# Kernel tuning notes

Measured on AMD Instinct MI355X. Metric: run time of the kernel, lower is better.

Reference implementation:

```python
import jax, jax.numpy as jnp
import numpy as np

# Config constants (mirrors VQConfig)
N_CODEBOOKS = 4
NUM_EMBS = 512
EMB_DIM = 32
NUM_LATENTS = 64
DECAY = 0.999
COMMITMENT_COST = 0.25
EPSILON = 1e-05
BATCH = 1024


def setup_inputs() -> dict:
    key = jax.random.key(0)
    k1, k2 = jax.random.split(key)
    x = jax.random.normal(k1, (BATCH, N_CODEBOOKS * EMB_DIM * NUM_LATENTS), dtype=jnp.float32)
    # embedding.uniform_(-1/M*5, 1/M*5)
    lim = 5.0 / NUM_EMBS
    embedding = jax.random.uniform(k2, (N_CODEBOOKS, NUM_EMBS, EMB_DIM), dtype=jnp.float32,
                                   minval=-lim, maxval=lim)
    ema_count = jnp.zeros((N_CODEBOOKS, NUM_EMBS), dtype=jnp.float32)
    ema_weight = embedding  # clone of embedding at init
    return {"x": x, "embedding": embedding, "ema_count": ema_count, "ema_weight": ema_weight}


def reference(x, embedding, ema_count, ema_weight):
    N, M, D = embedding.shape
    B = x.shape[0]
    L = x.shape[1] // (N * D)  # num_discrete_latents (H dim; W = 1)
    T = B * L  # flattened positions per codebook

    # x.view(B, N*D, L, 1).view(B, N, D, H, W).permute(1,0,3,4,2) -> [N,B,L,1,D]
    xr = x.reshape(B, N, D, L, 1).transpose(1, 0, 3, 4, 2)
    x_flat = jax.lax.stop_gradient(xr).reshape(N, T, D)

    e_sq = jnp.sum(embedding ** 2, axis=2)                       # [N, M]
    x_sq = jnp.sum(x_flat ** 2, axis=2, keepdims=True)           # [N, T, 1]
    xe = jnp.einsum('ntd,nmd->ntm', x_flat, embedding)           # [N, T, M]
    distances = e_sq[:, None, :] + x_sq - 2.0 * xe
    indices = jnp.argmin(distances, axis=-1)                     # [N, T] int

    # gather: quantized[n, t] = embedding[n, indices[n, t]]
    quantized = jnp.take_along_axis(embedding, indices[..., None], axis=1)  # [N,T,D]
    quantized_r = quantized.reshape(N, B, L, 1, D)

    # one-hot sums without materializing one-hot: scatter-add via segment_sum
    flat_idx = (indices + jnp.arange(N, dtype=indices.dtype)[:, None] * M).reshape(-1)
    counts = jax.ops.segment_sum(jnp.ones((N * T,), jnp.float32), flat_idx,
                                 num_segments=N * M).reshape(N, M)
    dw = jax.ops.segment_sum(x_flat.reshape(N * T, D), flat_idx,
                             num_segments=N * M).reshape(N, M, D)

    # EMA updates (training branch)
    new_ema_count = DECAY * ema_count + (1.0 - DECAY) * counts
    n_tot = jnp.sum(new_ema_count, axis=-1, keepdims=True)
    new_ema_count = (new_ema_count + EPSILON) / (n_tot + M * EPSILON) * n_tot
    new_ema_weight = DECAY * ema_weight + (1.0 - DECAY) * dw
    new_embedding = new_ema_weight / new_ema_count[..., None]

    # commitment loss + straight-through estimator
    e_latent_loss = jnp.mean((xr - jax.lax.stop_gradient(quantized_r)) ** 2)
    loss = COMMITMENT_COST * e_latent_loss
    quantized_st = jax.lax.stop_gradient(quantized_r) + xr - jax.lax.stop_gradient(xr)

    # perplexity
    avg_probs = counts / T                                       # [N, M]
    perplexity = jnp.exp(-jnp.sum(avg_probs * jnp.log(avg_probs + 1e-10), axis=-1))
    perplexity_sum = jnp.sum(perplexity)

    # [N,B,L,1,D] -> permute(1,0,4,2,3) -> [B,N,D,L,1] -> flatten
    z_q = quantized_st.transpose(1, 0, 4, 2, 3).reshape(B, N * D * L)
    indices_out = indices.reshape(N, B, L, 1).transpose(1, 0, 2, 3)  # [B,N,L,1]

    return (z_q, loss, perplexity_sum, indices_out,
            new_embedding, new_ema_count, new_ema_weight)
```

## Files before the change

### kernel.cpp

```cpp
#include <hip/hip_runtime.h>

#define NCB 4
#define M 512
#define D 32
#define L 64
#define B 1024
#define XS (NCB * D * L)
#define HALF_M 256

#define ZQ_OFF   0
#define LOSS_OFF 8388608
#define PERP_OFF 8388609
#define IDX_OFF  8388610
#define NEMB_OFF 8650754
#define NEC_OFF  8716290
#define NWE_OFF  8718338

#define WS_COUNTS 0
#define WS_DW     2048
#define WS_SSE    67584
#define WS_FLOATS (WS_SSE + 1)

#define NP_SUM32(sq, res) do {                                              \
    float r0=(sq)[0], r1=(sq)[1], r2=(sq)[2], r3=(sq)[3];                   \
    float r4=(sq)[4], r5=(sq)[5], r6=(sq)[6], r7=(sq)[7];                   \
    r0 += (sq)[8];  r1 += (sq)[9];  r2 += (sq)[10]; r3 += (sq)[11];         \
    r4 += (sq)[12]; r5 += (sq)[13]; r6 += (sq)[14]; r7 += (sq)[15];         \
    r0 += (sq)[16]; r1 += (sq)[17]; r2 += (sq)[18]; r3 += (sq)[19];         \
    r4 += (sq)[20]; r5 += (sq)[21]; r6 += (sq)[22]; r7 += (sq)[23];         \
    r0 += (sq)[24]; r1 += (sq)[25]; r2 += (sq)[26]; r3 += (sq)[27];         \
    r4 += (sq)[28]; r5 += (sq)[29]; r6 += (sq)[30]; r7 += (sq)[31];         \
    (res) = ((r0 + r1) + (r2 + r3)) + ((r4 + r5) + (r6 + r7));              \
} while (0)

__global__ __launch_bounds__(256) void vq_main(
    const float* __restrict__ x, const float* __restrict__ emb,
    float* __restrict__ out, float* __restrict__ ws)
{
#pragma clang fp contract(off)
    __shared__ float s_emb[HALF_M * D];
    __shared__ float s_esq[HALF_M];

    const int tid = threadIdx.x;
    const int lane = tid & 63;
    const int bid = blockIdx.x;
    const int n  = bid >> 7;
    const int t0 = (bid & 127) << 9;
    const float* __restrict__ embn = emb + n * (M * D);

    float xr[2][D];
    int tt[2];
#pragma unroll
    for (int j = 0; j < 2; ++j) {
        const int t = t0 + j * 256 + tid;
        tt[j] = t;
        const int b = t >> 6, l = t & 63;
        const float* xp = x + (size_t)b * XS + n * (D * L) + l;
#pragma unroll
        for (int d = 0; d < D; ++d) xr[j][d] = xp[d * L];
    }

    float xsq[2];
#pragma unroll
    for (int j = 0; j < 2; ++j) {
        float sq[D];
#pragma unroll
        for (int d = 0; d < D; ++d) sq[d] = xr[j][d] * xr[j][d];
        NP_SUM32(sq, xsq[j]);
    }

    float best[2] = {3.4e38f, 3.4e38f};
    int   bidx[2] = {0, 0};

    for (int half = 0; half < 2; ++half) {
        if (half) __syncthreads();
        const float4* src = (const float4*)(embn + half * HALF_M * D);
        float4* dst = (float4*)s_emb;
#pragma unroll
        for (int k = 0; k < 8; ++k) dst[tid + k * 256] = src[tid + k * 256];
        __syncthreads();
        {
            float sq[D];
#pragma unroll
            for (int d = 0; d < D; ++d) {
                const float e = s_emb[tid * D + d];
                sq[d] = e * e;
            }
            NP_SUM32(sq, s_esq[tid]);
        }
        __syncthreads();

        for (int mm = 0; mm < HALF_M; ++mm) {
            float ee[D];
            {
                const float4* e4 = (const float4*)(s_emb + mm * D);
#pragma unroll
                for (int q = 0; q < 8; ++q) {
                    const float4 v = e4[q];
                    ee[q*4+0] = v.x; ee[q*4+1] = v.y; ee[q*4+2] = v.z; ee[q*4+3] = v.w;
                }
            }
            const float es = s_esq[mm];
            const int m = half * HALF_M + mm;
#pragma unroll
            for (int j = 0; j < 2; ++j) {
                float l[4];
#pragma unroll
                for (int il = 0; il < 4; ++il) {
                    float c;
                    c = xr[j][12+il] * ee[12+il];
                    c = xr[j][ 8+il] * ee[ 8+il] + c;
                    c = xr[j][ 4+il] * ee[ 4+il] + c;
                    c = xr[j][ 0+il] * ee[ 0+il] + c;
                    c = xr[j][28+il] * ee[28+il] + c;
                    c = xr[j][24+il] * ee[24+il] + c;
                    c = xr[j][20+il] * ee[20+il] + c;
                    c = xr[j][16+il] * ee[16+il] + c;
                    l[il] = c;
                }
                const float xe   = (l[0] + l[1]) + (l[2] + l[3]);
                const float a1   = es + xsq[j];
                const float dist = a1 - 2.f * xe;
                if (dist < best[j]) { best[j] = dist; bidx[j] = m; }
            }
        }
    }

    float sse = 0.f;
#pragma unroll
    for (int j = 0; j < 2; ++j) {
        const int t = tt[j], b = t >> 6, l = t & 63;
        const float* q = embn + bidx[j] * D;
        float* zq = out + ZQ_OFF + (size_t)b * XS + n * (D * L) + l;
#pragma unroll
        for (int d = 0; d < D; ++d) {
            const float qv = q[d];
            zq[d * L] = qv;
            const float diff = xr[j][d] - qv;
            sse = fmaf(diff, diff, sse);
        }
        out[IDX_OFF + ((size_t)b * NCB + n) * L + l] = (float)bidx[j];
        unsafeAtomicAdd(&ws[WS_COUNTS + n * M + bidx[j]], 1.0f);
        float* dwp = ws + WS_DW + (size_t)(n * M + bidx[j]) * D;
#pragma unroll
        for (int d = 0; d < D; ++d) unsafeAtomicAdd(&dwp[d], xr[j][d]);
    }

#pragma unroll
    for (int off = 32; off > 0; off >>= 1) sse += __shfl_down(sse, off, 64);
    if (lane == 0) unsafeAtomicAdd(&ws[WS_SSE], sse);
}

__global__ __launch_bounds__(256) void vq_finalize(
    const float* __restrict__ ema_count, const float* __restrict__ ema_weight,
    const float* __restrict__ ws, float* __restrict__ out)
{
    const int n = blockIdx.x, tid = threadIdx.x;
    __shared__ float s_nec[M];
    __shared__ float s_red[16];

    float pre[2], tot = 0.f, ent = 0.f;
#pragma unroll
    for (int k = 0; k < 2; ++k) {
        const int m = tid + k * 256;
        const float c = ws[WS_COUNTS + n * M + m];
        pre[k] = 0.999f * ema_count[n * M + m] + 0.001f * c;
        tot += pre[k];
        const float p = c * (1.f / 65536.f);
        ent += p * logf(p + 1e-10f);
    }
#pragma unroll
    for (int off = 32; off > 0; off >>= 1) {
        tot += __shfl_down(tot, off, 64);
        ent += __shfl_down(ent, off, 64);
    }
    const int w = tid >> 6;
    if ((tid & 63) == 0) { s_red[w] = tot; s_red[8 + w] = ent; }
    __syncthreads();
    tot = s_red[0] + s_red[1] + s_red[2] + s_red[3];
    ent = s_red[8] + s_red[9] + s_red[10] + s_red[11];

    if (tid == 0) unsafeAtomicAdd(&out[PERP_OFF], expf(-ent));
    if (n == 0 && tid == 0) out[LOSS_OFF] = 0.25f * ws[WS_SSE] * (1.f / 8388608.f);

#pragma unroll
    for (int k = 0; k < 2; ++k) {
        const int m = tid + k * 256;
        const float nec = (pre[k] + 1e-5f) / (tot + M * 1e-5f) * tot;
        out[NEC_OFF + n * M + m] = nec;
        s_nec[m] = nec;
    }
    __syncthreads();

    for (int e = tid; e < M * D; e += 256) {
        const int m = e >> 5;
        const float wv = 0.999f * ema_weight[n * (M * D) + e] + 0.001f * ws[WS_DW + n * (M * D) + e];
        out[NWE_OFF + n * (M * D) + e] = wv;
        out[NEMB_OFF + n * (M * D) + e] = wv / s_nec[m];
    }
}

extern "C" void kernel_launch(void* const* d_in, const int* in_sizes, int n_in,
                              void* d_out, int out_size, void* d_ws, size_t ws_size,
                              hipStream_t stream) {
    const float* x          = (const float*)d_in[0];
    const float* embedding  = (const float*)d_in[1];
    const float* ema_count  = (const float*)d_in[2];
    const float* ema_weight = (const float*)d_in[3];
    float* out = (float*)d_out;
    float* ws  = (float*)d_ws;

    hipMemsetAsync(ws, 0, WS_FLOATS * sizeof(float), stream);
    hipMemsetAsync((char*)d_out + (size_t)LOSS_OFF * sizeof(float), 0, 2 * sizeof(float), stream);

    vq_main<<<dim3(512), dim3(256), 0, stream>>>(x, embedding, out, ws);
    vq_finalize<<<dim3(NCB), dim3(256), 0, stream>>>(ema_count, ema_weight, ws, out);
}
```

Measured before the change: 892.6 us.

## Use fast FMA distance search with top-two tracking and exact refinement of near-ties

Replaces the contract-off distance loop with an FMA-based score (||e||^2 - 2x·e, dropping the constant ||x||^2) and tracks both the best and second-best score per point. Points whose top two scores lie within a small epsilon are recomputed wave-cooperatively with the original exact arithmetic, keeping the argmin bit-compatible with the reference. Each thread now handles one point instead of two, the grid is doubled, the codebook is staged in quarters, and launch bounds request higher occupancy. All codebook norms are precomputed once into shared memory. The intent is to cut ALU work and raise occupancy, at the cost of occasional divergent refinement passes.

```diff
diff --git a/kernel.cpp b/kernel.cpp
--- a/kernel.cpp
+++ b/kernel.cpp
@@ -6,7 +6,7 @@
 #define L 64
 #define B 1024
 #define XS (NCB * D * L)
-#define HALF_M 256
+#define QM 128
 
 #define ZQ_OFF   0
 #define LOSS_OFF 8388608
@@ -20,6 +20,8 @@
 #define WS_DW     2048
 #define WS_SSE    67584
 #define WS_FLOATS (WS_SSE + 1)
+
+#define REFINE_EPS 1e-4f
 
 #define NP_SUM32(sq, res) do {                                              \
     float r0=(sq)[0], r1=(sq)[1], r2=(sq)[2], r3=(sq)[3];                   \
@@ -33,117 +35,149 @@
     (res) = ((r0 + r1) + (r2 + r3)) + ((r4 + r5) + (r6 + r7));              \
 } while (0)
 
-__global__ __launch_bounds__(256) void vq_main(
+__global__ __launch_bounds__(256, 4) void vq_main(
     const float* __restrict__ x, const float* __restrict__ emb,
     float* __restrict__ out, float* __restrict__ ws)
 {
 #pragma clang fp contract(off)
-    __shared__ float s_emb[HALF_M * D];
-    __shared__ float s_esq[HALF_M];
+    __shared__ float s_emb[QM * D];
+    __shared__ float s_esq[M];
 
     const int tid = threadIdx.x;
     const int lane = tid & 63;
     const int bid = blockIdx.x;
-    const int n  = bid >> 7;
-    const int t0 = (bid & 127) << 9;
+    const int n  = bid >> 8;
+    const int t  = ((bid & 255) << 8) + tid;
     const float* __restrict__ embn = emb + n * (M * D);
 
-    float xr[2][D];
-    int tt[2];
-#pragma unroll
-    for (int j = 0; j < 2; ++j) {
-        const int t = t0 + j * 256 + tid;
-        tt[j] = t;
-        const int b = t >> 6, l = t & 63;
+#pragma unroll
+    for (int k = 0; k < 2; ++k) {
+        const int r = tid + k * 256;
+        const float* ep = embn + r * D;
+        float sq[D];
+#pragma unroll
+        for (int d = 0; d < D; ++d) { const float e = ep[d]; sq[d] = e * e; }
+        NP_SUM32(sq, s_esq[r]);
+    }
+
+    const int b = t >> 6, l = t & 63;
+    float xr[D];
+    {
         const float* xp = x + (size_t)b * XS + n * (D * L) + l;
 #pragma unroll
-        for (int d = 0; d < D; ++d) xr[j][d] = xp[d * L];
-    }
-
-    float xsq[2];
-#pragma unroll
-    for (int j = 0; j < 2; ++j) {
+        for (int d = 0; d < D; ++d) xr[d] = xp[d * L];
+    }
+
+    float xsq;
+    {
         float sq[D];
 #pragma unroll
-        for (int d = 0; d < D; ++d) sq[d] = xr[j][d] * xr[j][d];
-        NP_SUM32(sq, xsq[j]);
-    }
-
-    float best[2] = {3.4e38f, 3.4e38f};
-    int   bidx[2] = {0, 0};
-
-    for (int half = 0; half < 2; ++half) {
-        if (half) __syncthreads();
-        const float4* src = (const float4*)(embn + half * HALF_M * D);
-        float4* dst = (float4*)s_emb;
-#pragma unroll
-        for (int k = 0; k < 8; ++k) dst[tid + k * 256] = src[tid + k * 256];
+        for (int d = 0; d < D; ++d) sq[d] = xr[d] * xr[d];
+        NP_SUM32(sq, xsq);
+    }
+
+    float best = 3.4e38f, secnd = 3.4e38f;
+    int   bi = 0;
+
+    for (int qtr = 0; qtr < 4; ++qtr) {
         __syncthreads();
         {
-            float sq[D];
-#pragma unroll
-            for (int d = 0; d < D; ++d) {
-                const float e = s_emb[tid * D + d];
-                sq[d] = e * e;
+            const float4* src = (const float4*)(embn + qtr * (QM * D));
+            float4* dst = (float4*)s_emb;
+#pragma unroll
+            for (int k = 0; k < 4; ++k) dst[tid + k * 256] = src[tid + k * 256];
+        }
+        __syncthreads();
+
+        for (int mm = 0; mm < QM; ++mm) {
+            const float4* e4 = (const float4*)(s_emb + mm * D);
+            const int m = qtr * QM + mm;
+            const float es = s_esq[m];
+            float a0 = 0.f, a1 = 0.f, a2 = 0.f, a3 = 0.f;
+#pragma unroll
+            for (int q = 0; q < 8; q += 4) {
+                const float4 v0 = e4[q], v1 = e4[q+1], v2 = e4[q+2], v3 = e4[q+3];
+                a0 = fmaf(v0.x, xr[q*4+ 0], a0); a0 = fmaf(v0.y, xr[q*4+ 1], a0);
+                a0 = fmaf(v0.z, xr[q*4+ 2], a0); a0 = fmaf(v0.w, xr[q*4+ 3], a0);
+                a1 = fmaf(v1.x, xr[q*4+ 4], a1); a1 = fmaf(v1.y, xr[q*4+ 5], a1);
+                a1 = fmaf(v1.z, xr[q*4+ 6], a1); a1 = fmaf(v1.w, xr[q*4+ 7], a1);
+                a2 = fmaf(v2.x, xr[q*4+ 8], a2); a2 = fmaf(v2.y, xr[q*4+ 9], a2);
+                a2 = fmaf(v2.z, xr[q*4+10], a2); a2 = fmaf(v2.w, xr[q*4+11], a2);
+                a3 = fmaf(v3.x, xr[q*4+12], a3); a3 = fmaf(v3.y, xr[q*4+13], a3);
+                a3 = fmaf(v3.z, xr[q*4+14], a3); a3 = fmaf(v3.w, xr[q*4+15], a3);
             }
-            NP_SUM32(sq, s_esq[tid]);
-        }
-        __syncthreads();
-
-        for (int mm = 0; mm < HALF_M; ++mm) {
-            float ee[D];
-            {
-                const float4* e4 = (const float4*)(s_emb + mm * D);
+            const float s = fmaf(-2.f, ((a0 + a1) + (a2 + a3)), es);
+            const bool lt = s < best;
+            secnd = lt ? best : fminf(secnd, s);
+            best  = lt ? s : best;
+            bi    = lt ? m : bi;
+        }
+    }
+
+    {
+        unsigned long long mask = __ballot(secnd - best < REFINE_EPS);
+        while (mask) {
+            const int src = __ffsll(mask) - 1;
+            mask &= mask - 1;
+            float xb[D];
+#pragma unroll
+            for (int d = 0; d < D; ++d) xb[d] = __shfl(xr[d], src, 64);
+            const float xsb = __shfl(xsq, src, 64);
+            float bs = 3.4e38f; int bm = M;
+            for (int mb = 0; mb < 8; ++mb) {
+                const int m = mb * 64 + lane;
+                const float4* e4 = (const float4*)(embn + m * D);
+                float ee[D];
 #pragma unroll
                 for (int q = 0; q < 8; ++q) {
                     const float4 v = e4[q];
                     ee[q*4+0] = v.x; ee[q*4+1] = v.y; ee[q*4+2] = v.z; ee[q*4+3] = v.w;
                 }
-            }
-            const float es = s_esq[mm];
-            const int m = half * HALF_M + mm;
-#pragma unroll
-            for (int j = 0; j < 2; ++j) {
-                float l[4];
+                float lnk[4];
 #pragma unroll
                 for (int il = 0; il < 4; ++il) {
                     float c;
-                    c = xr[j][12+il] * ee[12+il];
-                    c = xr[j][ 8+il] * ee[ 8+il] + c;
-                    c = xr[j][ 4+il] * ee[ 4+il] + c;
-                    c = xr[j][ 0+il] * ee[ 0+il] + c;
-                    c = xr[j][28+il] * ee[28+il] + c;
-                    c = xr[j][24+il] * ee[24+il] + c;
-                    c = xr[j][20+il] * ee[20+il] + c;
-                    c = xr[j][16+il] * ee[16+il] + c;
-                    l[il] = c;
+                    c = xb[12+il] * ee[12+il];
+                    c = xb[ 8+il] * ee[ 8+il] + c;
+                    c = xb[ 4+il] * ee[ 4+il] + c;
+                    c = xb[ 0+il] * ee[ 0+il] + c;
+                    c = xb[28+il] * ee[28+il] + c;
+                    c = xb[24+il] * ee[24+il] + c;
+                    c = xb[20+il] * ee[20+il] + c;
+                    c = xb[16+il] * ee[16+il] + c;
+                    lnk[il] = c;
                 }
-                const float xe   = (l[0] + l[1]) + (l[2] + l[3]);
-                const float a1   = es + xsq[j];
+                const float xe   = (lnk[0] + lnk[1]) + (lnk[2] + lnk[3]);
+                const float a1   = s_esq[m] + xsb;
                 const float dist = a1 - 2.f * xe;
-                if (dist < best[j]) { best[j] = dist; bidx[j] = m; }
+                if (dist < bs || (dist == bs && m < bm)) { bs = dist; bm = m; }
             }
+#pragma unroll
+            for (int off = 32; off > 0; off >>= 1) {
+                const float os = __shfl_xor(bs, off, 64);
+                const int   om = __shfl_xor(bm, off, 64);
+                if (os < bs || (os == bs && om < bm)) { bs = os; bm = om; }
+            }
+            if (lane == src) bi = bm;
         }
     }
 
     float sse = 0.f;
-#pragma unroll
-    for (int j = 0; j < 2; ++j) {
-        const int t = tt[j], b = t >> 6, l = t & 63;
-        const float* q = embn + bidx[j] * D;
+    {
+        const float* q = embn + bi * D;
         float* zq = out + ZQ_OFF + (size_t)b * XS + n * (D * L) + l;
 #pragma unroll
         for (int d = 0; d < D; ++d) {
             const float qv = q[d];
             zq[d * L] = qv;
-            const float diff = xr[j][d] - qv;
+            const float diff = xr[d] - qv;
             sse = fmaf(diff, diff, sse);
         }
-        out[IDX_OFF + ((size_t)b * NCB + n) * L + l] = (float)bidx[j];
-        unsafeAtomicAdd(&ws[WS_COUNTS + n * M + bidx[j]], 1.0f);
-        float* dwp = ws + WS_DW + (size_t)(n * M + bidx[j]) * D;
-#pragma unroll
-        for (int d = 0; d < D; ++d) unsafeAtomicAdd(&dwp[d], xr[j][d]);
+        out[IDX_OFF + ((size_t)b * NCB + n) * L + l] = (float)bi;
+        unsafeAtomicAdd(&ws[WS_COUNTS + n * M + bi], 1.0f);
+        float* dwp = ws + WS_DW + (size_t)(n * M + bi) * D;
+#pragma unroll
+        for (int d = 0; d < D; ++d) unsafeAtomicAdd(&dwp[d], xr[d]);
     }
 
 #pragma unroll
@@ -213,6 +247,6 @@
     hipMemsetAsync(ws, 0, WS_FLOATS * sizeof(float), stream);
     hipMemsetAsync((char*)d_out + (size_t)LOSS_OFF * sizeof(float), 0, 2 * sizeof(float), stream);
 
-    vq_main<<<dim3(512), dim3(256), 0, stream>>>(x, embedding, out, ws);
+    vq_main<<<dim3(1024), dim3(256), 0, stream>>>(x, embedding, out, ws);
     vq_finalize<<<dim3(NCB), dim3(256), 0, stream>>>(ema_count, ema_weight, ws, out);
 }
```

Result: no change. 882.5 us (-1.1%).

## Use fast FMA scoring with near-tie exact refinement and full codebook in LDS

Applied to the files above, without the earlier changes.

The distance search now drops the per-row x-squared term and scores each code with FMA chains, tracking best and second-best. When the gap between them is under a threshold, the lane is rescored wave-cooperatively using the original exact non-contracted arithmetic, so the argmin matches the reference. The full codebook is loaded into shared memory once, and the embedding norms are precomputed by a separate kernel, which removes the half-split reloads and extra barriers. This costs more LDS per block and adds a divergent refinement path plus an extra launch.

```diff
diff --git a/kernel.cpp b/kernel.cpp
--- a/kernel.cpp
+++ b/kernel.cpp
@@ -6,7 +6,6 @@
 #define L 64
 #define B 1024
 #define XS (NCB * D * L)
-#define HALF_M 256
 
 #define ZQ_OFF   0
 #define LOSS_OFF 8388608
@@ -19,7 +18,10 @@
 #define WS_COUNTS 0
 #define WS_DW     2048
 #define WS_SSE    67584
-#define WS_FLOATS (WS_SSE + 1)
+#define WS_ESQ    67585
+#define WS_FLOATS (WS_ESQ + NCB * M)
+
+#define REFINE_EPS 1e-4f
 
 #define NP_SUM32(sq, res) do {                                              \
     float r0=(sq)[0], r1=(sq)[1], r2=(sq)[2], r3=(sq)[3];                   \
@@ -33,13 +35,27 @@
     (res) = ((r0 + r1) + (r2 + r3)) + ((r4 + r5) + (r6 + r7));              \
 } while (0)
 
-__global__ __launch_bounds__(256) void vq_main(
+__global__ __launch_bounds__(256) void vq_esq(
+    const float* __restrict__ emb, float* __restrict__ ws)
+{
+#pragma clang fp contract(off)
+    const int r = blockIdx.x * 256 + threadIdx.x;
+    const float* ep = emb + (size_t)r * D;
+    float sq[D];
+#pragma unroll
+    for (int d = 0; d < D; ++d) { const float e = ep[d]; sq[d] = e * e; }
+    float res;
+    NP_SUM32(sq, res);
+    ws[WS_ESQ + r] = res;
+}
+
+__global__ __launch_bounds__(256, 2) void vq_main(
     const float* __restrict__ x, const float* __restrict__ emb,
+    const float* __restrict__ esq,
     float* __restrict__ out, float* __restrict__ ws)
 {
 #pragma clang fp contract(off)
-    __shared__ float s_emb[HALF_M * D];
-    __shared__ float s_esq[HALF_M];
+    __shared__ float s_emb[M * D];
 
     const int tid = threadIdx.x;
     const int lane = tid & 63;
@@ -47,6 +63,14 @@
     const int n  = bid >> 7;
     const int t0 = (bid & 127) << 9;
     const float* __restrict__ embn = emb + n * (M * D);
+    const float* __restrict__ esqn = esq + n * M;
+
+    {
+        const float4* src = (const float4*)embn;
+        float4* dst = (float4*)s_emb;
+#pragma unroll
+        for (int k = 0; k < 16; ++k) dst[tid + k * 256] = src[tid + k * 256];
+    }
 
     float xr[2][D];
     int tt[2];
@@ -69,60 +93,100 @@
         NP_SUM32(sq, xsq[j]);
     }
 
-    float best[2] = {3.4e38f, 3.4e38f};
+    __syncthreads();
+
+    float best[2] = {3.4e38f, 3.4e38f}, secnd[2] = {3.4e38f, 3.4e38f};
     int   bidx[2] = {0, 0};
 
-    for (int half = 0; half < 2; ++half) {
-        if (half) __syncthreads();
-        const float4* src = (const float4*)(embn + half * HALF_M * D);
-        float4* dst = (float4*)s_emb;
-#pragma unroll
-        for (int k = 0; k < 8; ++k) dst[tid + k * 256] = src[tid + k * 256];
-        __syncthreads();
-        {
-            float sq[D];
-#pragma unroll
-            for (int d = 0; d < D; ++d) {
-                const float e = s_emb[tid * D + d];
-                sq[d] = e * e;
-            }
-            NP_SUM32(sq, s_esq[tid]);
+#define SCORE(mrow, e) do {                                                   \
+        const float es = esqn[(mrow)];                 \
+        _Pragma("unroll")                                                     \
+        for (int j = 0; j < 2; ++j) {                                         \
+            float a0 = 0.f, a1 = 0.f, a2 = 0.f, a3 = 0.f;                     \
+            _Pragma("unroll")                                                 \
+            for (int q = 0; q < 8; q += 4) {                                  \
+                const float4 v0 = (e)[q],   v1 = (e)[q+1];                    \
+                const float4 v2 = (e)[q+2], v3 = (e)[q+3];                    \
+                a0 = fmaf(v0.x, xr[j][q*4+ 0], a0); a0 = fmaf(v0.y, xr[j][q*4+ 1], a0); \
+                a0 = fmaf(v0.z, xr[j][q*4+ 2], a0); a0 = fmaf(v0.w, xr[j][q*4+ 3], a0); \
+                a1 = fmaf(v1.x, xr[j][q*4+ 4], a1); a1 = fmaf(v1.y, xr[j][q*4+ 5], a1); \
+                a1 = fmaf(v1.z, xr[j][q*4+ 6], a1); a1 = fmaf(v1.w, xr[j][q*4+ 7], a1); \
+                a2 = fmaf(v2.x, xr[j][q*4+ 8], a2); a2 = fmaf(v2.y, xr[j][q*4+ 9], a2); \
+                a2 = fmaf(v2.z, xr[j][q*4+10], a2); a2 = fmaf(v2.w, xr[j][q*4+11], a2); \
+                a3 = fmaf(v3.x, xr[j][q*4+12], a3); a3 = fmaf(v3.y, xr[j][q*4+13], a3); \
+                a3 = fmaf(v3.z, xr[j][q*4+14], a3); a3 = fmaf(v3.w, xr[j][q*4+15], a3); \
+            }                                                                 \
+            const float s = fmaf(-2.f, ((a0 + a1) + (a2 + a3)), es);          \
+            const bool lt = s < best[j];                                      \
+            secnd[j] = lt ? best[j] : fminf(secnd[j], s);                     \
+            best[j]  = lt ? s : best[j];                                      \
+            bidx[j]  = lt ? (mrow) : bidx[j];                                 \
+        }                                                                     \
+    } while (0)
+
+    {
+        const float4* e4 = (const float4*)s_emb;
+        float4 eA[8], eB[8];
+#pragma unroll
+        for (int q = 0; q < 8; ++q) eA[q] = e4[q];
+        for (int m = 0; m < M; m += 2) {
+#pragma unroll
+            for (int q = 0; q < 8; ++q) eB[q] = e4[(m + 1) * 8 + q];
+            SCORE(m, eA);
+            const int mn = (m + 2) & (M - 1);
+#pragma unroll
+            for (int q = 0; q < 8; ++q) eA[q] = e4[mn * 8 + q];
+            SCORE(m + 1, eB);
         }
-        __syncthreads();
-
-        for (int mm = 0; mm < HALF_M; ++mm) {
-            float ee[D];
-            {
-                const float4* e4 = (const float4*)(s_emb + mm * D);
+    }
+#undef SCORE
+
+#pragma unroll
+    for (int j = 0; j < 2; ++j) {
+        unsigned long long mask = __ballot(secnd[j] - best[j] < REFINE_EPS);
+        while (mask) {
+            const int src = __ffsll(mask) - 1;
+            mask &= mask - 1;
+            float xb[D];
+#pragma unroll
+            for (int d = 0; d < D; ++d) xb[d] = __shfl(xr[j][d], src, 64);
+            const float xsb = __shfl(xsq[j], src, 64);
+            float bs = 3.4e38f; int bm = M;
+            for (int mb = 0; mb < 8; ++mb) {
+                const int m = mb * 64 + lane;
+                const float4* r4 = (const float4*)(s_emb + m * D);
+                float ee[D];
 #pragma unroll
                 for (int q = 0; q < 8; ++q) {
-                    const float4 v = e4[q];
+                    const float4 v = r4[q];
                     ee[q*4+0] = v.x; ee[q*4+1] = v.y; ee[q*4+2] = v.z; ee[q*4+3] = v.w;
                 }
-            }
-            const float es = s_esq[mm];
-            const int m = half * HALF_M + mm;
-#pragma unroll
-            for (int j = 0; j < 2; ++j) {
-                float l[4];
+                float lnk[4];
 #pragma unroll
                 for (int il = 0; il < 4; ++il) {
                     float c;
-                    c = xr[j][12+il] * ee[12+il];
-                    c = xr[j][ 8+il] * ee[ 8+il] + c;
-                    c = xr[j][ 4+il] * ee[ 4+il] + c;
-                    c = xr[j][ 0+il] * ee[ 0+il] + c;
-                    c = xr[j][28+il] * ee[28+il] + c;
-                    c = xr[j][24+il] * ee[24+il] + c;
-                    c = xr[j][20+il] * ee[20+il] + c;
-                    c = xr[j][16+il] * ee[16+il] + c;
-                    l[il] = c;
+                    c = xb[12+il] * ee[12+il];
+                    c = xb[ 8+il] * ee[ 8+il] + c;
+                    c = xb[ 4+il] * ee[ 4+il] + c;
+                    c = xb[ 0+il] * ee[ 0+il] + c;
+                    c = xb[28+il] * ee[28+il] + c;
+                    c = xb[24+il] * ee[24+il] + c;
+                    c = xb[20+il] * ee[20+il] + c;
+                    c = xb[16+il] * ee[16+il] + c;
+                    lnk[il] = c;
                 }
-                const float xe   = (l[0] + l[1]) + (l[2] + l[3]);
-                const float a1   = es + xsq[j];
-                const float dist = a1 - 2.f * xe;
-                if (dist < best[j]) { best[j] = dist; bidx[j] = m; }
+                const float xe   = (lnk[0] + lnk[1]) + (lnk[2] + lnk[3]);
+                const float a1v  = esqn[m] + xsb;
+                const float dist = a1v - 2.f * xe;
+                if (dist < bs || (dist == bs && m < bm)) { bs = dist; bm = m; }
             }
+#pragma unroll
+            for (int off = 32; off > 0; off >>= 1) {
+                const float os = __shfl_xor(bs, off, 64);
+                const int   om = __shfl_xor(bm, off, 64);
+                if (os < bs || (os == bs && om < bm)) { bs = os; bm = om; }
+            }
+            if (lane == src) bidx[j] = bm;
         }
     }
 
@@ -130,7 +194,7 @@
 #pragma unroll
     for (int j = 0; j < 2; ++j) {
         const int t = tt[j], b = t >> 6, l = t & 63;
-        const float* q = embn + bidx[j] * D;
+        const float* q = s_emb + bidx[j] * D;
         float* zq = out + ZQ_OFF + (size_t)b * XS + n * (D * L) + l;
 #pragma unroll
         for (int d = 0; d < D; ++d) {
@@ -210,9 +274,10 @@
     float* out = (float*)d_out;
     float* ws  = (float*)d_ws;
 
-    hipMemsetAsync(ws, 0, WS_FLOATS * sizeof(float), stream);
+    hipMemsetAsync(ws, 0, (WS_SSE + 1) * sizeof(float), stream);
     hipMemsetAsync((char*)d_out + (size_t)LOSS_OFF * sizeof(float), 0, 2 * sizeof(float), stream);
 
-    vq_main<<<dim3(512), dim3(256), 0, stream>>>(x, embedding, out, ws);
+    vq_esq<<<dim3(NCB * M / 256), dim3(256), 0, stream>>>(embedding, ws);
+    vq_main<<<dim3(512), dim3(256), 0, stream>>>(x, embedding, ws + WS_ESQ, out, ws);
     vq_finalize<<<dim3(NCB), dim3(256), 0, stream>>>(ema_count, ema_weight, ws, out);
 }
```

New measurement: 851.6 us. 4.6% less time.
